# Kernel optimization log

Measured on AMD Instinct MI355X. Metric: run time of the kernel, lower is better.

Reference implementation:

```python
import jax, jax.numpy as jnp
import numpy as np

R_MAX = 5.0
NUM_BASIS = 8
CUTOFF_P = 6
N_LAYERS = 3
C = 64          # hidden_mul / channels of irreps_conv_out (64x0e+64x1o)
Z = 4           # element_number
AVG_DEG = 32.0  # num-neighbor normalization (E/N)
SQRT3 = 1.7320508075688772
SQRT2 = 1.4142135623730951


def _radial_embedding(r):
    # Bessel basis * polynomial cutoff (RadialEdgeEmbedding)
    rs = jnp.maximum(r, 1e-9)
    n = jnp.arange(1, NUM_BASIS + 1, dtype=r.dtype)  # (B,)
    bessel = jnp.sqrt(2.0 / R_MAX) * jnp.sin(n * jnp.pi * rs[:, None] / R_MAX) / rs[:, None]
    x = r / R_MAX
    p = float(CUTOFF_P)
    fc = (1.0
          - (p + 1.0) * (p + 2.0) / 2.0 * x ** CUTOFF_P
          + p * (p + 2.0) * x ** (CUTOFF_P + 1)
          - p * (p + 1.0) / 2.0 * x ** (CUTOFF_P + 2))
    fc = jnp.where(x < 1.0, fc, 0.0)
    return bessel * fc[:, None]  # (E, NUM_BASIS)


def setup_inputs() -> dict:
    key = jax.random.key(0)
    ks = jax.random.split(key, 20)
    N, E, B = 16000, 512000, 16
    atom_type = jax.random.randint(ks[0], (N,), 0, Z)
    # atoms in a 4A box so most edge lengths fall inside r_max=5
    atom_pos = jax.random.uniform(ks[1], (N, 3), dtype=jnp.float32) * 4.0
    edge_src = jax.random.randint(ks[2], (E,), 0, N)
    edge_dst = jax.random.randint(ks[3], (E,), 0, N)
    edge_cell_shift = jnp.zeros((E, 3), jnp.float32)
    cell = jnp.tile(jnp.eye(3, dtype=jnp.float32) * 10.0, (B, 1, 1)) \
        + 0.01 * jax.random.normal(ks[4], (B, 3, 3), jnp.float32)
    image_index = jax.random.randint(ks[5], (N,), 0, B)
    g = lambda k, s, fan: jax.random.normal(k, s, jnp.float32) / np.sqrt(fan)
    return {
        'atom_type': atom_type, 'atom_pos': atom_pos,
        'edge_src': edge_src, 'edge_dst': edge_dst,
        'edge_cell_shift': edge_cell_shift, 'cell': cell, 'image_index': image_index,
        'w_lin_in': g(ks[6], (Z, C), Z),
        'mlp_w1': g(ks[7], (N_LAYERS, NUM_BASIS, 64), NUM_BASIS),
        'mlp_b1': jnp.zeros((N_LAYERS, 64), jnp.float32),
        'mlp_w2': g(ks[8], (N_LAYERS, 64, 5 * C), 64),
        'w_self_s': g(ks[9], (N_LAYERS, C, C), C),
        'w_self_v': g(ks[10], (N_LAYERS, C, C), C),
        'w_gate': g(ks[11], (N_LAYERS, C, C), C),
        'w_lin1': g(ks[12], (C, 16), C),
        'w_lin2': g(ks[13], (16, 1), 16),
    }


def reference(atom_type, atom_pos, edge_src, edge_dst, edge_cell_shift, cell,
              image_index, w_lin_in, mlp_w1, mlp_b1, mlp_w2,
              w_self_s, w_self_v, w_gate, w_lin1, w_lin2):
    N = atom_pos.shape[0]
    # edge vectors with periodic cell shift
    edge_vec = atom_pos[edge_dst] - atom_pos[edge_src]
    edge_vec = edge_vec + jnp.einsum('ni,nij->nj', edge_cell_shift,
                                     cell.reshape(-1, 3, 3)[image_index[edge_src]])
    r = jnp.linalg.norm(edge_vec, axis=1)                      # (E,)
    unit = edge_vec / jnp.maximum(r, 1e-9)[:, None]
    # spherical harmonics lmax=1, component normalization: y0=1 (implicit), y1=sqrt(3)*unit
    y1 = SQRT3 * unit                                           # (E, 3)
    emb = _radial_embedding(r)                                  # (E, NUM_BASIS)

    # one-hot embedding + input linear (one-hot is all 0e -> scalar channels only)
    onehot = jax.nn.one_hot(atom_type, Z, dtype=atom_pos.dtype)
    s = onehot @ w_lin_in                                       # (N, C) l=0 features
    v = jnp.zeros((N, C, 3), atom_pos.dtype)                    # (N, C, 3) l=1 features

    inv_sqrt_deg = 1.0 / np.sqrt(AVG_DEG)
    for L in range(N_LAYERS):
        # radial MLP -> per-edge per-channel tensor-product path weights
        w = jax.nn.silu(emb @ mlp_w1[L] + mlp_b1[L]) @ mlp_w2[L]  # (E, 5C)
        w1, w2, w3, w4, w5 = jnp.split(w, 5, axis=1)              # (E, C) each
        s_src = s[edge_src]                                       # (E, C)
        v_src = v[edge_src]                                       # (E, C, 3)
        vdoty = jnp.einsum('ecx,ex->ec', v_src, y1)
        # CG tensor-product paths (l<=1):
        m_s = w1 * s_src + w2 * vdoty / SQRT3                     # 0x0->0, 1x1->0
        m_v = (w3[:, :, None] * s_src[:, :, None] * y1[:, None, :]      # 0x1->1
               + w4[:, :, None] * v_src                                  # 1x0->1
               + w5[:, :, None] * jnp.cross(v_src, y1[:, None, :]) / SQRT2)  # 1x1->1
        agg_s = jax.ops.segment_sum(m_s, edge_dst, num_segments=N) * inv_sqrt_deg
        agg_v = jax.ops.segment_sum(m_v, edge_dst, num_segments=N) * inv_sqrt_deg
        # gated self-interaction + resnet
        gate = jax.nn.sigmoid(agg_s @ w_gate[L])                  # (N, C)
        s = s + jax.nn.silu(agg_s @ w_self_s[L])
        v = v + jnp.einsum('ncx,cd->ndx', agg_v, w_self_v[L]) * gate[:, :, None]

    # o3.Linear to 16x0e then 1x0e (only scalar channels map to 0e outputs)
    atomic_energy = (s @ w_lin1) @ w_lin2                         # (N, 1)
    atomic_energy = atomic_energy * 1.0                           # atomic_scale
    return atomic_energy
```

## Files before the change

kernel.cpp:

```cpp
#include <hip/hip_runtime.h>
#include <hip/hip_fp16.h>
#include <math.h>

#define NUM_BASIS 8
#define SQRT3 1.7320508075688772f
#define SQRT2 1.4142135623730951f
#define INV_SQRT_DEG 0.17677669529663687f
#define PI_F 3.14159265358979323846f

typedef _Float16 half8 __attribute__((ext_vector_type(8)));
typedef float float4v __attribute__((ext_vector_type(4)));

__device__ __forceinline__ float sigmoidf_(float x) { return 1.0f / (1.0f + __expf(-x)); }
__device__ __forceinline__ float siluf_(float x) { return x * sigmoidf_(x); }

__device__ __forceinline__ void unp2(unsigned u, float& a, float& b) {
    __half2 h = *reinterpret_cast<__half2*>(&u);
    float2 f = __half22float2(h);
    a = f.x; b = f.y;
}
__device__ __forceinline__ unsigned pk2(float a, float b) {
    __half2 h = __floats2half2_rn(a, b);
    return *reinterpret_cast<unsigned*>(&h);
}

__global__ __launch_bounds__(256) void count_deg(
    const int* __restrict__ dst, int* __restrict__ deg, int E)
{
    int base = (blockIdx.x * blockDim.x + threadIdx.x) * 4;
    if (base + 3 < E) {
        int4 d4 = *(const int4*)(dst + base);
        atomicAdd(&deg[d4.x], 1);
        atomicAdd(&deg[d4.y], 1);
        atomicAdd(&deg[d4.z], 1);
        atomicAdd(&deg[d4.w], 1);
    } else {
        for (int e = base; e < E; e++) atomicAdd(&deg[dst[e]], 1);
    }
}

__global__ __launch_bounds__(1024) void scan_deg(
    const int* __restrict__ deg, int* __restrict__ cursor, int N)
{
    __shared__ int wsum[16];
    __shared__ int carry_s, tot_s;
    int tid = threadIdx.x;
    int wid = tid >> 6, lane = tid & 63;
    if (tid == 0) carry_s = 0;
    __syncthreads();
    for (int base = 0; base < N; base += 16384) {
        int i0 = base + tid * 16;
        int v[16];
        int sum = 0;
        #pragma unroll
        for (int k = 0; k < 16; k++) {
            int i = i0 + k;
            v[k] = (i < N) ? deg[i] : 0;
            sum += v[k];
        }
        int incl = sum;
        #pragma unroll
        for (int off = 1; off < 64; off <<= 1) {
            int t = __shfl_up(incl, off);
            if (lane >= off) incl += t;
        }
        if (lane == 63) wsum[wid] = incl;
        __syncthreads();
        if (wid == 0 && lane < 16) {
            int wv = wsum[lane];
            int wincl = wv;
            #pragma unroll
            for (int off = 1; off < 16; off <<= 1) {
                int t = __shfl_up(wincl, off);
                if (lane >= off) wincl += t;
            }
            wsum[lane] = wincl - wv;
            if (lane == 15) tot_s = wincl;
        }
        __syncthreads();
        int carry = carry_s;
        int run = carry + wsum[wid] + incl - sum;
        #pragma unroll
        for (int k = 0; k < 16; k++) {
            int i = i0 + k;
            if (i < N) cursor[i] = run;
            run += v[k];
        }
        __syncthreads();
        if (tid == 0) carry_s = carry + tot_s;
        __syncthreads();
    }
}

__global__ __launch_bounds__(256) void edge_pre_scatter(
    const float* __restrict__ pos, const int* __restrict__ src,
    const int* __restrict__ dst, const float* __restrict__ cs,
    const float* __restrict__ cell, const int* __restrict__ img,
    int* __restrict__ cursor, _Float16* __restrict__ emb,
    uint2* __restrict__ y14, int2* __restrict__ sdp, int E)
{
    int e = blockIdx.x * blockDim.x + threadIdx.x;
    if (e >= E) return;
    int si = src[e], di = dst[e];
    int slot = atomicAdd(&cursor[di], 1);
    sdp[slot] = make_int2(si, di);
    float vx = pos[di*3+0] - pos[si*3+0];
    float vy = pos[di*3+1] - pos[si*3+1];
    float vz = pos[di*3+2] - pos[si*3+2];
    float c0 = cs[(size_t)e*3+0], c1 = cs[(size_t)e*3+1], c2 = cs[(size_t)e*3+2];
    const float* M = cell + (size_t)img[si] * 9;
    vx += c0*M[0] + c1*M[3] + c2*M[6];
    vy += c0*M[1] + c1*M[4] + c2*M[7];
    vz += c0*M[2] + c1*M[5] + c2*M[8];
    float r  = sqrtf(vx*vx + vy*vy + vz*vz);
    float rs = fmaxf(r, 1e-9f);
    float inv = 1.0f / rs;
    uint2 yv;
    yv.x = pk2(SQRT3*vx*inv, SQRT3*vy*inv);
    yv.y = pk2(SQRT3*vz*inv, 0.f);
    y14[slot] = yv;
    float x = r * (1.0f / 5.0f);
    float x2 = x*x, x6 = x2*x2*x2;
    float fc = 1.0f - 28.0f*x6 + 48.0f*x6*x - 21.0f*x6*x2;
    if (x >= 1.0f) fc = 0.0f;
    float pre = sqrtf(2.0f / 5.0f) * inv * fc;
    float t = PI_F * rs * (1.0f / 5.0f);
    half8 ev;
    #pragma unroll
    for (int n = 1; n <= NUM_BASIS; n++)
        ev[n-1] = (_Float16)(pre * __sinf((float)n * t));
    *(half8*)(emb + (size_t)slot*NUM_BASIS) = ev;
}

__global__ __launch_bounds__(256) void prep_weights(
    const float* __restrict__ W2, _Float16* __restrict__ w2f,
    const float* __restrict__ Wg, const float* __restrict__ Ws,
    const float* __restrict__ Wv, _Float16* __restrict__ wgtf,
    const float* __restrict__ Wl1, const float* __restrict__ Wl2,
    float* __restrict__ wl12)
{
    int idx = blockIdx.x * blockDim.x + threadIdx.x;
    if (idx < 64) {
        float a = 0.f;
        #pragma unroll
        for (int j = 0; j < 16; j++) a = fmaf(Wl1[idx*16 + j], Wl2[j], a);
        wl12[idx] = a;
    }
    if (idx < 3 * 20480) {
        int L  = idx / 20480;
        int r  = idx % 20480;
        int cg = r / 5120;
        int r2 = r % 5120;
        int p  = r2 / 1024;
        int r3 = r2 % 1024;
        int kh = r3 / 512;
        int r4 = r3 % 512;
        int lane = r4 / 8;
        int j  = r4 % 8;
        int k = kh*32 + (lane >> 4)*8 + j;
        int n = p*64 + cg*16 + (lane & 15);
        float val = W2[(size_t)L*20480 + k*320 + n];
        if (p == 1)      val *= 0.5773502691896258f;
        else if (p == 4) val *= 0.7071067811865476f;
        w2f[idx] = (_Float16)val;
    } else if (idx < 3*20480 + 3*3*4096) {
        int idx2 = idx - 3*20480;
        int L   = idx2 / 12288;
        int rem = idx2 % 12288;
        int mat = rem / 4096;
        int r2  = rem % 4096;
        int cg  = r2 / 1024;
        int r3  = r2 % 1024;
        int kh  = r3 / 512;
        int r4  = r3 % 512;
        int lane = r4 / 8;
        int j   = r4 % 8;
        int k = kh*32 + (lane >> 4)*8 + j;
        int n = cg*16 + (lane & 15);
        const float* src = (mat == 0) ? Wg : (mat == 1) ? Ws : Wv;
        wgtf[idx2] = (_Float16)src[(size_t)L*4096 + k*64 + n];
    }
}

__global__ __launch_bounds__(256) void mlp1_pre(
    const _Float16* __restrict__ emb, const float* __restrict__ W1,
    const float* __restrict__ B1, _Float16* __restrict__ hA, int E)
{
    int g    = blockIdx.x * blockDim.x + threadIdx.x;
    int kb   = (g & 7) * 8;
    int es   = g >> 3;
    int estr = (gridDim.x * blockDim.x) >> 3;
    float wv[8][8];
    #pragma unroll
    for (int jj = 0; jj < 8; jj++) {
        float4 a = *(const float4*)(W1 + jj*64 + kb);
        float4 b = *(const float4*)(W1 + jj*64 + kb + 4);
        wv[jj][0]=a.x; wv[jj][1]=a.y; wv[jj][2]=a.z; wv[jj][3]=a.w;
        wv[jj][4]=b.x; wv[jj][5]=b.y; wv[jj][6]=b.z; wv[jj][7]=b.w;
    }
    float bv[8];
    {
        float4 a = *(const float4*)(B1 + kb);
        float4 b = *(const float4*)(B1 + kb + 4);
        bv[0]=a.x; bv[1]=a.y; bv[2]=a.z; bv[3]=a.w;
        bv[4]=b.x; bv[5]=b.y; bv[6]=b.z; bv[7]=b.w;
    }
    for (int e = es; e < E; e += estr) {
        half8 ev = *(const half8*)(emb + (size_t)e*8);
        float hv[8];
        #pragma unroll
        for (int j = 0; j < 8; j++) hv[j] = bv[j];
        #pragma unroll
        for (int jj = 0; jj < 8; jj++) {
            float em = (float)ev[jj];
            #pragma unroll
            for (int j = 0; j < 8; j++)
                hv[j] = fmaf(em, wv[jj][j], hv[j]);
        }
        half8 out;
        #pragma unroll
        for (int j = 0; j < 8; j++) out[j] = (_Float16)siluf_(hv[j]);
        *(half8*)(hA + (size_t)e*64 + kb) = out;
    }
}

__device__ __forceinline__ void mlp1_afrag(
    const _Float16* __restrict__ emb, const float* __restrict__ W1,
    const float* __restrict__ B1, int eA, int q, half8 afrag[2])
{
    half8 ev = *(const half8*)(emb + (size_t)eA*8);
    float em[8];
    #pragma unroll
    for (int j = 0; j < 8; j++) em[j] = (float)ev[j];
    #pragma unroll
    for (int kh = 0; kh < 2; kh++) {
        int kb = kh*32 + q*8;
        float hv[8];
        float4 b0 = *(const float4*)(B1 + kb);
        float4 b1 = *(const float4*)(B1 + kb + 4);
        hv[0]=b0.x; hv[1]=b0.y; hv[2]=b0.z; hv[3]=b0.w;
        hv[4]=b1.x; hv[5]=b1.y; hv[6]=b1.z; hv[7]=b1.w;
        #pragma unroll
        for (int jj = 0; jj < 8; jj++) {
            float4 wa = *(const float4*)(W1 + jj*64 + kb);
            float4 wb = *(const float4*)(W1 + jj*64 + kb + 4);
            hv[0] = fmaf(em[jj], wa.x, hv[0]);
            hv[1] = fmaf(em[jj], wa.y, hv[1]);
            hv[2] = fmaf(em[jj], wa.z, hv[2]);
            hv[3] = fmaf(em[jj], wa.w, hv[3]);
            hv[4] = fmaf(em[jj], wb.x, hv[4]);
            hv[5] = fmaf(em[jj], wb.y, hv[5]);
            hv[6] = fmaf(em[jj], wb.z, hv[6]);
            hv[7] = fmaf(em[jj], wb.w, hv[7]);
        }
        #pragma unroll
        for (int j = 0; j < 8; j++)
            afrag[kh][j] = (_Float16)siluf_(hv[j]);
    }
}

template<bool PRE>
__global__ __launch_bounds__(256) void edge_msg_mfma_l0(
    const _Float16* __restrict__ emb, const _Float16* __restrict__ hA,
    const uint2* __restrict__ y14, const int2* __restrict__ sdp,
    const int* __restrict__ type, const float* __restrict__ wlin,
    const float* __restrict__ W1, const float* __restrict__ B1,
    const _Float16* __restrict__ w2f,
    float* __restrict__ aggs, float* __restrict__ aggx,
    float* __restrict__ aggy, float* __restrict__ aggz, int E)
{
    __shared__ _Float16 w2s[8192];
    {
        half8* dstv = (half8*)w2s;
        const half8* srcv = (const half8*)w2f;
        #pragma unroll
        for (int k = 0; k < 4; k++) {
            int t  = threadIdx.x + k*256;
            int cg = t >> 8;
            int r  = t & 255;
            int pp = r >> 7;
            int rk = r & 127;
            dstv[t] = srcv[cg*640 + pp*256 + rk];
        }
    }
    __syncthreads();

    int wave  = (blockIdx.x * blockDim.x + threadIdx.x) >> 6;
    int lane  = threadIdx.x & 63;
    int wbase = wave * 16;
    if (wbase >= E) return;
    int q   = lane >> 4;
    int col = lane & 15;

    half8 afrag[2];
    if (PRE) {
        const _Float16* hp = hA + (size_t)(wbase + col)*64 + q*8;
        afrag[0] = *(const half8*)(hp);
        afrag[1] = *(const half8*)(hp + 32);
    }

    int eb = wbase + q*4;
    int d[4], tt[4];
    float y1x[4], y1y[4], y1z[4];
    #pragma unroll
    for (int r = 0; r < 4; r++) {
        int2 sv = sdp[eb + r];
        tt[r] = type[sv.x];
        d[r]  = sv.y;
        uint2 yv = y14[eb + r];
        float dummy;
        unp2(yv.x, y1x[r], y1y[r]);
        unp2(yv.y, y1z[r], dummy);
    }

    if (!PRE) mlp1_afrag(emb, W1, B1, wbase + col, q, afrag);

    int dnq = __shfl_down(d[0], 16);
    int nd3 = (q == 3) ? -1 : dnq;
    int df = d[0], dl = d[3];
    bool U = (df == dl);
    int dlp = __shfl_up(dl, 16);
    bool link = (q > 0) && (dlp == df);

    #pragma unroll
    for (int cg = 0; cg < 4; cg++) {
        float4v a1 = {0,0,0,0}, a3 = {0,0,0,0};
        const _Float16* wbp = w2s + ((size_t)cg*2048) + (size_t)lane*8;
        {
            half8 b10 = *(const half8*)(wbp + 0*512);
            half8 b11 = *(const half8*)(wbp + 1*512);
            half8 b30 = *(const half8*)(wbp + 2*512);
            half8 b31 = *(const half8*)(wbp + 3*512);
            a1 = __builtin_amdgcn_mfma_f32_16x16x32_f16(afrag[0], b10, a1, 0, 0, 0);
            a1 = __builtin_amdgcn_mfma_f32_16x16x32_f16(afrag[1], b11, a1, 0, 0, 0);
            a3 = __builtin_amdgcn_mfma_f32_16x16x32_f16(afrag[0], b30, a3, 0, 0, 0);
            a3 = __builtin_amdgcn_mfma_f32_16x16x32_f16(afrag[1], b31, a3, 0, 0, 0);
        }
        int c = cg*16 + col;

        float ms[4], mx[4], my[4], mz[4];
        #pragma unroll
        for (int r = 0; r < 4; r++) {
            float s = wlin[tt[r]*64 + c];
            float w3s = a3[r] * s;
            ms[r] = a1[r] * s;
            mx[r] = w3s * y1x[r];
            my[r] = w3s * y1y[r];
            mz[r] = w3s * y1z[r];
        }
        #pragma unroll
        for (int r = 1; r < 4; r++) {
            if (d[r] == d[r-1]) {
                ms[r] += ms[r-1]; mx[r] += mx[r-1];
                my[r] += my[r-1]; mz[r] += mz[r-1];
            }
        }
        float Cs = 0.f, Cx = 0.f, Cy = 0.f, Cz = 0.f;
        #pragma unroll
        for (int it = 0; it < 3; it++) {
            float es = ms[3] + (U ? Cs : 0.f);
            float ex = mx[3] + (U ? Cx : 0.f);
            float ey = my[3] + (U ? Cy : 0.f);
            float ez = mz[3] + (U ? Cz : 0.f);
            float ts = __shfl_up(es, 16);
            float tx = __shfl_up(ex, 16);
            float ty = __shfl_up(ey, 16);
            float tz = __shfl_up(ez, 16);
            Cs = link ? ts : 0.f; Cx = link ? tx : 0.f;
            Cy = link ? ty : 0.f; Cz = link ? tz : 0.f;
        }
        bool hr = true;
        #pragma unroll
        for (int r = 0; r < 4; r++) {
            if (r > 0) hr = hr && (d[r] == d[r-1]);
            float fs = ms[r] + (hr ? Cs : 0.f);
            float fx = mx[r] + (hr ? Cx : 0.f);
            float fy = my[r] + (hr ? Cy : 0.f);
            float fz = mz[r] + (hr ? Cz : 0.f);
            int ndx = (r < 3) ? d[r+1] : nd3;
            if (ndx != d[r] && d[r] >= 0) {
                size_t ai = (size_t)d[r]*64 + c;
                atomicAdd(aggs + ai, fs);
                atomicAdd(aggx + ai, fx);
                atomicAdd(aggy + ai, fy);
                atomicAdd(aggz + ai, fz);
            }
        }
    }
}

__device__ __forceinline__ void process_half(
    const _Float16* __restrict__ w2s, const half8 afrag[2],
    const uint2 pf[4][2], const int d[4], int nd3, bool U, bool link,
    bool live, const float* y1x, const float* y1y, const float* y1z,
    int cgh, int col,
    float* __restrict__ aggs, float* __restrict__ aggx,
    float* __restrict__ aggy, float* __restrict__ aggz)
{
    int lane = threadIdx.x & 63;
    #pragma unroll
    for (int cgl = 0; cgl < 2; cgl++) {
        float4v acc[5];
        #pragma unroll
        for (int p = 0; p < 5; p++) acc[p] = (float4v){0.f, 0.f, 0.f, 0.f};
        const _Float16* wbp = w2s + ((size_t)cgl*5120) + (size_t)lane*8;
        #pragma unroll
        for (int p = 0; p < 5; p++) {
            half8 bf0 = *(const half8*)(wbp + ((size_t)(p*2 + 0))*512);
            half8 bf1 = *(const half8*)(wbp + ((size_t)(p*2 + 1))*512);
            acc[p] = __builtin_amdgcn_mfma_f32_16x16x32_f16(afrag[0], bf0, acc[p], 0, 0, 0);
            acc[p] = __builtin_amdgcn_mfma_f32_16x16x32_f16(afrag[1], bf1, acc[p], 0, 0, 0);
        }
        int c = (cgh*2 + cgl)*16 + col;

        float ms[4], mx[4], my[4], mz[4];
        #pragma unroll
        for (int r = 0; r < 4; r++) {
            float fsx, fvx, fvy, fvz;
            unp2(pf[r][cgl].x, fsx, fvx);
            unp2(pf[r][cgl].y, fvy, fvz);
            float yx = y1x[r], yy = y1y[r], yz = y1z[r];
            float w1 = acc[0][r], w2 = acc[1][r], w3 = acc[2][r];
            float w4 = acc[3][r], w5 = acc[4][r];
            float vdoty = fvx*yx + fvy*yy + fvz*yz;
            ms[r] = fmaf(w1, fsx, w2*vdoty);
            float w3s = w3*fsx;
            float cx = fvy*yz - fvz*yy;
            float cy = fvz*yx - fvx*yz;
            float cz = fvx*yy - fvy*yx;
            mx[r] = fmaf(w3s, yx, fmaf(w4, fvx, w5*cx));
            my[r] = fmaf(w3s, yy, fmaf(w4, fvy, w5*cy));
            mz[r] = fmaf(w3s, yz, fmaf(w4, fvz, w5*cz));
        }
        #pragma unroll
        for (int r = 1; r < 4; r++) {
            if (d[r] == d[r-1]) {
                ms[r] += ms[r-1]; mx[r] += mx[r-1];
                my[r] += my[r-1]; mz[r] += mz[r-1];
            }
        }
        float Cs = 0.f, Cx = 0.f, Cy = 0.f, Cz = 0.f;
        #pragma unroll
        for (int it = 0; it < 3; it++) {
            float es = ms[3] + (U ? Cs : 0.f);
            float ex = mx[3] + (U ? Cx : 0.f);
            float ey = my[3] + (U ? Cy : 0.f);
            float ez = mz[3] + (U ? Cz : 0.f);
            float ts = __shfl_up(es, 16);
            float tx = __shfl_up(ex, 16);
            float ty = __shfl_up(ey, 16);
            float tz = __shfl_up(ez, 16);
            Cs = link ? ts : 0.f; Cx = link ? tx : 0.f;
            Cy = link ? ty : 0.f; Cz = link ? tz : 0.f;
        }
        bool hr = true;
        #pragma unroll
        for (int r = 0; r < 4; r++) {
            if (r > 0) hr = hr && (d[r] == d[r-1]);
            float fs = ms[r] + (hr ? Cs : 0.f);
            float fx = mx[r] + (hr ? Cx : 0.f);
            float fy = my[r] + (hr ? Cy : 0.f);
            float fz = mz[r] + (hr ? Cz : 0.f);
            int ndx = (r < 3) ? d[r+1] : nd3;
            if (ndx != d[r] && d[r] >= 0 && live) {
                size_t ai = (size_t)d[r]*64 + c;
                atomicAdd(aggs + ai, fs);
                atomicAdd(aggx + ai, fx);
                atomicAdd(aggy + ai, fy);
                atomicAdd(aggz + ai, fz);
            }
        }
    }
}

template<bool PRE>
__global__ __launch_bounds__(256) void edge_msg_mfma(
    const _Float16* __restrict__ emb, const _Float16* __restrict__ hA,
    const uint2* __restrict__ y14, const int2* __restrict__ sdp,
    const uint2* __restrict__ nf,
    const float* __restrict__ W1, const float* __restrict__ B1,
    const _Float16* __restrict__ w2f,
    float* __restrict__ aggs, float* __restrict__ aggx,
    float* __restrict__ aggy, float* __restrict__ aggz, int E)
{
    __shared__ _Float16 w2s[10240];
    {
        half8* dstv = (half8*)w2s;
        const half8* srcv = (const half8*)w2f;
        #pragma unroll
        for (int k = 0; k < 5; k++)
            dstv[threadIdx.x + k*256] = srcv[threadIdx.x + k*256];
    }
    __syncthreads();

    int wave  = (blockIdx.x * blockDim.x + threadIdx.x) >> 6;
    int lane  = threadIdx.x & 63;
    int wbase = wave * 16;
    bool live = wbase < E;
    int wb2   = live ? wbase : 0;
    int q   = lane >> 4;
    int col = lane & 15;

    half8 afrag[2];
    if (PRE) {
        const _Float16* hp = hA + (size_t)(wb2 + col)*64 + q*8;
        afrag[0] = *(const half8*)(hp);
        afrag[1] = *(const half8*)(hp + 32);
    }

    int eb = wb2 + q*4;
    int d[4], si[4];
    float y1x[4], y1y[4], y1z[4];
    #pragma unroll
    for (int r = 0; r < 4; r++) {
        int2 sv = sdp[eb + r];
        si[r] = sv.x;
        d[r]  = sv.y;
        uint2 yv = y14[eb + r];
        float dummy;
        unp2(yv.x, y1x[r], y1y[r]);
        unp2(yv.y, y1z[r], dummy);
    }

    uint2 pf[4][2];
    #pragma unroll
    for (int r = 0; r < 4; r++) {
        size_t nb = (size_t)si[r] * 64 + col;
        pf[r][0] = nf[nb];
        pf[r][1] = nf[nb + 16];
    }

    if (!PRE) mlp1_afrag(emb, W1, B1, wb2 + col, q, afrag);

    int dnq = __shfl_down(d[0], 16);
    int nd3 = (q == 3) ? -1 : dnq;
    int df = d[0], dl = d[3];
    bool U = (df == dl);
    int dlp = __shfl_up(dl, 16);
    bool link = (q > 0) && (dlp == df);

    process_half(w2s, afrag, pf, d, nd3, U, link, live,
                 y1x, y1y, y1z, 0, col, aggs, aggx, aggy, aggz);

    #pragma unroll
    for (int r = 0; r < 4; r++) {
        size_t nb = (size_t)si[r] * 64 + 32 + col;
        pf[r][0] = nf[nb];
        pf[r][1] = nf[nb + 16];
    }

    asm volatile("s_waitcnt lgkmcnt(0)" ::: "memory");
    __builtin_amdgcn_s_barrier();
    asm volatile("" ::: "memory");

    {
        half8* dstv = (half8*)w2s;
        const half8* srcv = (const half8*)w2f + 1280;
        #pragma unroll
        for (int k = 0; k < 5; k++)
            dstv[threadIdx.x + k*256] = srcv[threadIdx.x + k*256];
    }

    asm volatile("s_waitcnt lgkmcnt(0)" ::: "memory");
    __builtin_amdgcn_s_barrier();
    asm volatile("" ::: "memory");

    process_half(w2s, afrag, pf, d, nd3, U, link, live,
                 y1x, y1y, y1z, 1, col, aggs, aggx, aggy, aggz);
}

__global__ __launch_bounds__(256) void node_update_mfma(
    uint2* __restrict__ nf,
    float* __restrict__ aggs, float* __restrict__ aggx,
    float* __restrict__ aggy, float* __restrict__ aggz,
    const _Float16* __restrict__ wgtf,
    const int* __restrict__ type, const float* __restrict__ wlin,
    const float* __restrict__ wl12,
    float* __restrict__ out, int first, int do_out, int N)
{
    __shared__ _Float16 wgs[12288];
    {
        half8* dstv = (half8*)wgs;
        const half8* srcv = (const half8*)wgtf;
        #pragma unroll
        for (int k = 0; k < 6; k++)
            dstv[threadIdx.x + k*256] = srcv[threadIdx.x + k*256];
    }

    int wave  = (blockIdx.x * blockDim.x + threadIdx.x) >> 6;
    int lane  = threadIdx.x & 63;
    int wbase = wave * 16;
    bool active = wbase < N;
    int q = lane >> 4, col = lane & 15;

    int nodeA = active ? (wbase + col) : 0;
    if (nodeA >= N) nodeA = N - 1;
    size_t nb = (size_t)nodeA * 64 + q * 8;
    half8 af0[2], af1[2], af2[2], af3[2];
    #pragma unroll
    for (int kh = 0; kh < 2; kh++) {
        const float* p0 = aggs + nb + kh*32;
        const float* p1 = aggx + nb + kh*32;
        const float* p2 = aggy + nb + kh*32;
        const float* p3 = aggz + nb + kh*32;
        float4 a0 = *(const float4*)p0, b0 = *(const float4*)(p0+4);
        float4 a1 = *(const float4*)p1, b1 = *(const float4*)(p1+4);
        float4 a2 = *(const float4*)p2, b2 = *(const float4*)(p2+4);
        float4 a3 = *(const float4*)p3, b3 = *(const float4*)(p3+4);
        af0[kh][0]=(_Float16)(a0.x*INV_SQRT_DEG); af0[kh][1]=(_Float16)(a0.y*INV_SQRT_DEG);
        af0[kh][2]=(_Float16)(a0.z*INV_SQRT_DEG); af0[kh][3]=(_Float16)(a0.w*INV_SQRT_DEG);
        af0[kh][4]=(_Float16)(b0.x*INV_SQRT_DEG); af0[kh][5]=(_Float16)(b0.y*INV_SQRT_DEG);
        af0[kh][6]=(_Float16)(b0.z*INV_SQRT_DEG); af0[kh][7]=(_Float16)(b0.w*INV_SQRT_DEG);
        af1[kh][0]=(_Float16)(a1.x*INV_SQRT_DEG); af1[kh][1]=(_Float16)(a1.y*INV_SQRT_DEG);
        af1[kh][2]=(_Float16)(a1.z*INV_SQRT_DEG); af1[kh][3]=(_Float16)(a1.w*INV_SQRT_DEG);
        af1[kh][4]=(_Float16)(b1.x*INV_SQRT_DEG); af1[kh][5]=(_Float16)(b1.y*INV_SQRT_DEG);
        af1[kh][6]=(_Float16)(b1.z*INV_SQRT_DEG); af1[kh][7]=(_Float16)(b1.w*INV_SQRT_DEG);
        af2[kh][0]=(_Float16)(a2.x*INV_SQRT_DEG); af2[kh][1]=(_Float16)(a2.y*INV_SQRT_DEG);
        af2[kh][2]=(_Float16)(a2.z*INV_SQRT_DEG); af2[kh][3]=(_Float16)(a2.w*INV_SQRT_DEG);
        af2[kh][4]=(_Float16)(b2.x*INV_SQRT_DEG); af2[kh][5]=(_Float16)(b2.y*INV_SQRT_DEG);
        af2[kh][6]=(_Float16)(b2.z*INV_SQRT_DEG); af2[kh][7]=(_Float16)(b2.w*INV_SQRT_DEG);
        af3[kh][0]=(_Float16)(a3.x*INV_SQRT_DEG); af3[kh][1]=(_Float16)(a3.y*INV_SQRT_DEG);
        af3[kh][2]=(_Float16)(a3.z*INV_SQRT_DEG); af3[kh][3]=(_Float16)(a3.w*INV_SQRT_DEG);
        af3[kh][4]=(_Float16)(b3.x*INV_SQRT_DEG); af3[kh][5]=(_Float16)(b3.y*INV_SQRT_DEG);
        af3[kh][6]=(_Float16)(b3.z*INV_SQRT_DEG); af3[kh][7]=(_Float16)(b3.w*INV_SQRT_DEG);
    }

    int tt[4];
    #pragma unroll
    for (int r = 0; r < 4; r++) {
        int nd = wbase + q*4 + r;
        tt[r] = type[(active && nd < N) ? nd : 0];
    }

    __syncthreads();

    float epart[4] = {0.f, 0.f, 0.f, 0.f};

    #pragma unroll
    for (int cg = 0; cg < 4; cg++) {
        const _Float16* bp = wgs + (size_t)lane * 8;
        half8 bg0 = *(const half8*)(bp + ((size_t)((0*4 + cg)*2 + 0))*512);
        half8 bg1 = *(const half8*)(bp + ((size_t)((0*4 + cg)*2 + 1))*512);
        half8 bs0 = *(const half8*)(bp + ((size_t)((1*4 + cg)*2 + 0))*512);
        half8 bs1 = *(const half8*)(bp + ((size_t)((1*4 + cg)*2 + 1))*512);
        half8 bv0 = *(const half8*)(bp + ((size_t)((2*4 + cg)*2 + 0))*512);
        half8 bv1 = *(const half8*)(bp + ((size_t)((2*4 + cg)*2 + 1))*512);
        float4v ag = {0,0,0,0}, as = {0,0,0,0};
        float4v ox = {0,0,0,0}, oy = {0,0,0,0}, oz = {0,0,0,0};
        ag = __builtin_amdgcn_mfma_f32_16x16x32_f16(af0[0], bg0, ag, 0, 0, 0);
        ag = __builtin_amdgcn_mfma_f32_16x16x32_f16(af0[1], bg1, ag, 0, 0, 0);
        as = __builtin_amdgcn_mfma_f32_16x16x32_f16(af0[0], bs0, as, 0, 0, 0);
        as = __builtin_amdgcn_mfma_f32_16x16x32_f16(af0[1], bs1, as, 0, 0, 0);
        ox = __builtin_amdgcn_mfma_f32_16x16x32_f16(af1[0], bv0, ox, 0, 0, 0);
        ox = __builtin_amdgcn_mfma_f32_16x16x32_f16(af1[1], bv1, ox, 0, 0, 0);
        oy = __builtin_amdgcn_mfma_f32_16x16x32_f16(af2[0], bv0, oy, 0, 0, 0);
        oy = __builtin_amdgcn_mfma_f32_16x16x32_f16(af2[1], bv1, oy, 0, 0, 0);
        oz = __builtin_amdgcn_mfma_f32_16x16x32_f16(af3[0], bv0, oz, 0, 0, 0);
        oz = __builtin_amdgcn_mfma_f32_16x16x32_f16(af3[1], bv1, oz, 0, 0, 0);

        if (!active) continue;
        int c = cg*16 + col;
        float wlc = wl12[c];
        #pragma unroll
        for (int r = 0; r < 4; r++) {
            int nd = wbase + q*4 + r;
            bool wr = nd < N;
            size_t ni = (size_t)nd*64 + c;
            float sx, vx, vy, vz;
            if (first) {
                sx = wlin[tt[r]*64 + c];
                vx = 0.f; vy = 0.f; vz = 0.f;
            } else {
                uint2 cur = nf[wr ? ni : 0];
                unp2(cur.x, sx, vx);
                unp2(cur.y, vy, vz);
            }
            float gate = sigmoidf_(ag[r]);
            sx += siluf_(as[r]);
            vx += ox[r] * gate;
            vy += oy[r] * gate;
            vz += oz[r] * gate;
            if (wr) {
                uint2 nv;
                nv.x = pk2(sx, vx);
                nv.y = pk2(vy, vz);
                nf[ni] = nv;
                aggs[ni] = 0.f;
                aggx[ni] = 0.f;
                aggy[ni] = 0.f;
                aggz[ni] = 0.f;
                epart[r] = fmaf(sx, wlc, epart[r]);
            }
        }
    }
    if (do_out && active) {
        #pragma unroll
        for (int r = 0; r < 4; r++) {
            float e = epart[r];
            e += __shfl_xor(e, 1);
            e += __shfl_xor(e, 2);
            e += __shfl_xor(e, 4);
            e += __shfl_xor(e, 8);
            int nd = wbase + q*4 + r;
            if (col == 0 && nd < N) out[nd] = e;
        }
    }
}

extern "C" void kernel_launch(void* const* d_in, const int* in_sizes, int n_in,
                              void* d_out, int out_size, void* d_ws, size_t ws_size,
                              hipStream_t stream)
{
    const int*   atom_type = (const int*)  d_in[0];
    const float* pos       = (const float*)d_in[1];
    const int*   src       = (const int*)  d_in[2];
    const int*   dst       = (const int*)  d_in[3];
    const float* cs        = (const float*)d_in[4];
    const float* cell      = (const float*)d_in[5];
    const int*   img       = (const int*)  d_in[6];
    const float* wlin_in   = (const float*)d_in[7];
    const float* mw1       = (const float*)d_in[8];
    const float* mb1       = (const float*)d_in[9];
    const float* mw2       = (const float*)d_in[10];
    const float* wss       = (const float*)d_in[11];
    const float* wsv       = (const float*)d_in[12];
    const float* wg        = (const float*)d_in[13];
    const float* wl1       = (const float*)d_in[14];
    const float* wl2       = (const float*)d_in[15];
    int N = in_sizes[0];
    int E = in_sizes[2];

    char* w = (char*)d_ws;
    _Float16* emb = (_Float16*)w; w += (size_t)E * 8 * sizeof(_Float16);
    uint2*  y14  = (uint2*)w;  w += (size_t)E * sizeof(uint2);
    int2*   sdp  = (int2*)w;   w += (size_t)E * sizeof(int2);
    uint2*  nf   = (uint2*)w;  w += (size_t)N * 64 * sizeof(uint2);
    float*  agg  = (float*)w;  w += (size_t)N * 64 * 4 * sizeof(float);
    _Float16* w2f  = (_Float16*)w; w += (size_t)3 * 20480 * sizeof(_Float16);
    _Float16* wgtf = (_Float16*)w; w += (size_t)3 * 3 * 4096 * sizeof(_Float16);
    float*  wl12 = (float*)w;  w += 64 * sizeof(float);
    int*    deg  = (int*)w;    w += (size_t)N * sizeof(int);
    int*    curs = (int*)w;    w += (size_t)N * sizeof(int);

    size_t used   = (size_t)(w - (char*)d_ws);
    size_t hbytes = (size_t)E * 64 * sizeof(_Float16);
    int nh = (ws_size >= used + hbytes) ? 1 : 0;
    _Float16* hbuf = (_Float16*)w;

    size_t NC = (size_t)N * 64;
    float* aggs = agg;
    float* aggx = agg + NC;
    float* aggy = agg + 2*NC;
    float* aggz = agg + 3*NC;

    hipMemsetAsync(deg, 0, (size_t)N * sizeof(int), stream);
    hipMemsetAsync(agg, 0, NC * 4 * sizeof(float), stream);
    count_deg<<<(E/4 + 255) / 256, 256, 0, stream>>>(dst, deg, E);
    scan_deg<<<1, 1024, 0, stream>>>(deg, curs, N);
    int prep_n = 3*20480 + 3*3*4096;
    prep_weights<<<(prep_n + 255) / 256, 256, 0, stream>>>(
        mw2, w2f, wg, wss, wsv, wgtf, wl1, wl2, wl12);
    edge_pre_scatter<<<(E + 255) / 256, 256, 0, stream>>>(
        pos, src, dst, cs, cell, img, curs, emb, y14, sdp, E);

    int eblocks = (E + 63) / 64;
    int nblocks = (N + 63) / 64;
    int pblocks = 2048;

    if (nh) {
        mlp1_pre<<<pblocks, 256, 0, stream>>>(emb, mw1, mb1, hbuf, E);
        edge_msg_mfma_l0<true><<<eblocks, 256, 0, stream>>>(
            emb, hbuf, y14, sdp, atom_type, wlin_in,
            mw1, mb1, w2f, aggs, aggx, aggy, aggz, E);
    } else {
        edge_msg_mfma_l0<false><<<eblocks, 256, 0, stream>>>(
            emb, nullptr, y14, sdp, atom_type, wlin_in,
            mw1, mb1, w2f, aggs, aggx, aggy, aggz, E);
    }
    node_update_mfma<<<nblocks, 256, 0, stream>>>(
        nf, aggs, aggx, aggy, aggz, wgtf, atom_type, wlin_in, wl12,
        (float*)d_out, 1, 0, N);

    for (int L = 1; L < 3; L++) {
        if (nh) {
            mlp1_pre<<<pblocks, 256, 0, stream>>>(
                emb, mw1 + L * 8 * 64, mb1 + L * 64, hbuf, E);
            edge_msg_mfma<true><<<eblocks, 256, 0, stream>>>(
                emb, hbuf, y14, sdp, nf,
                mw1 + L * 8 * 64, mb1 + L * 64, w2f + (size_t)L * 20480,
                aggs, aggx, aggy, aggz, E);
        } else {
            edge_msg_mfma<false><<<eblocks, 256, 0, stream>>>(
                emb, nullptr, y14, sdp, nf,
                mw1 + L * 8 * 64, mb1 + L * 64, w2f + (size_t)L * 20480,
                aggs, aggx, aggy, aggz, E);
        }
        node_update_mfma<<<nblocks, 256, 0, stream>>>(
            nf, aggs, aggx, aggy, aggz,
            wgtf + (size_t)L * 12288, atom_type, wlin_in, wl12,
            (float*)d_out, 0, (L == 2) ? 1 : 0, N);
    }
}
```

Measured before the change: 464.9 us.

## Fuse weight prep into scan, overlap next-layer MLP1 with node update, uniform-dst fast path

Merges the degree scan and weight preparation into one launch, with extra blocks doing the weight conversion. The next layer's MLP1 precompute is now run by extra blocks of the node-update kernel, so it overlaps with node work and needs no separate launch. In the edge message kernels, when all 16 edges of a wave share one destination, a cross-lane shuffle reduction does a single atomic per channel instead of the segmented reduction. The overlap depends on the hidden-buffer reuse being ordered correctly, and the uniform-destination check adds a wave vote to every wave.

```diff
diff --git a/kernel.cpp b/kernel.cpp
--- a/kernel.cpp
+++ b/kernel.cpp
@@ -39,9 +39,59 @@
     }
 }
 
-__global__ __launch_bounds__(1024) void scan_deg(
-    const int* __restrict__ deg, int* __restrict__ cursor, int N)
-{
+__global__ __launch_bounds__(1024) void scan_prep(
+    const int* __restrict__ deg, int* __restrict__ cursor, int N,
+    const float* __restrict__ W2, _Float16* __restrict__ w2f,
+    const float* __restrict__ Wg, const float* __restrict__ Ws,
+    const float* __restrict__ Wv, _Float16* __restrict__ wgtf,
+    const float* __restrict__ Wl1, const float* __restrict__ Wl2,
+    float* __restrict__ wl12)
+{
+    if (blockIdx.x != 0) {
+        int idx = ((int)blockIdx.x - 1) * 1024 + (int)threadIdx.x;
+        if (idx < 64) {
+            float a = 0.f;
+            #pragma unroll
+            for (int j = 0; j < 16; j++) a = fmaf(Wl1[idx*16 + j], Wl2[j], a);
+            wl12[idx] = a;
+        }
+        if (idx < 3 * 20480) {
+            int L  = idx / 20480;
+            int r  = idx % 20480;
+            int cg = r / 5120;
+            int r2 = r % 5120;
+            int p  = r2 / 1024;
+            int r3 = r2 % 1024;
+            int kh = r3 / 512;
+            int r4 = r3 % 512;
+            int lane = r4 / 8;
+            int j  = r4 % 8;
+            int k = kh*32 + (lane >> 4)*8 + j;
+            int n = p*64 + cg*16 + (lane & 15);
+            float val = W2[(size_t)L*20480 + k*320 + n];
+            if (p == 1)      val *= 0.5773502691896258f;
+            else if (p == 4) val *= 0.7071067811865476f;
+            w2f[idx] = (_Float16)val;
+        } else if (idx < 3*20480 + 3*3*4096) {
+            int idx2 = idx - 3*20480;
+            int L   = idx2 / 12288;
+            int rem = idx2 % 12288;
+            int mat = rem / 4096;
+            int r2  = rem % 4096;
+            int cg  = r2 / 1024;
+            int r3  = r2 % 1024;
+            int kh  = r3 / 512;
+            int r4  = r3 % 512;
+            int lane = r4 / 8;
+            int j   = r4 % 8;
+            int k = kh*32 + (lane >> 4)*8 + j;
+            int n = cg*16 + (lane & 15);
+            const float* src = (mat == 0) ? Wg : (mat == 1) ? Ws : Wv;
+            wgtf[idx2] = (_Float16)src[(size_t)L*4096 + k*64 + n];
+        }
+        return;
+    }
+
     __shared__ int wsum[16];
     __shared__ int carry_s, tot_s;
     int tid = threadIdx.x;
@@ -132,64 +182,14 @@
     *(half8*)(emb + (size_t)slot*NUM_BASIS) = ev;
 }
 
-__global__ __launch_bounds__(256) void prep_weights(
-    const float* __restrict__ W2, _Float16* __restrict__ w2f,
-    const float* __restrict__ Wg, const float* __restrict__ Ws,
-    const float* __restrict__ Wv, _Float16* __restrict__ wgtf,
-    const float* __restrict__ Wl1, const float* __restrict__ Wl2,
-    float* __restrict__ wl12)
-{
-    int idx = blockIdx.x * blockDim.x + threadIdx.x;
-    if (idx < 64) {
-        float a = 0.f;
-        #pragma unroll
-        for (int j = 0; j < 16; j++) a = fmaf(Wl1[idx*16 + j], Wl2[j], a);
-        wl12[idx] = a;
-    }
-    if (idx < 3 * 20480) {
-        int L  = idx / 20480;
-        int r  = idx % 20480;
-        int cg = r / 5120;
-        int r2 = r % 5120;
-        int p  = r2 / 1024;
-        int r3 = r2 % 1024;
-        int kh = r3 / 512;
-        int r4 = r3 % 512;
-        int lane = r4 / 8;
-        int j  = r4 % 8;
-        int k = kh*32 + (lane >> 4)*8 + j;
-        int n = p*64 + cg*16 + (lane & 15);
-        float val = W2[(size_t)L*20480 + k*320 + n];
-        if (p == 1)      val *= 0.5773502691896258f;
-        else if (p == 4) val *= 0.7071067811865476f;
-        w2f[idx] = (_Float16)val;
-    } else if (idx < 3*20480 + 3*3*4096) {
-        int idx2 = idx - 3*20480;
-        int L   = idx2 / 12288;
-        int rem = idx2 % 12288;
-        int mat = rem / 4096;
-        int r2  = rem % 4096;
-        int cg  = r2 / 1024;
-        int r3  = r2 % 1024;
-        int kh  = r3 / 512;
-        int r4  = r3 % 512;
-        int lane = r4 / 8;
-        int j   = r4 % 8;
-        int k = kh*32 + (lane >> 4)*8 + j;
-        int n = cg*16 + (lane & 15);
-        const float* src = (mat == 0) ? Wg : (mat == 1) ? Ws : Wv;
-        wgtf[idx2] = (_Float16)src[(size_t)L*4096 + k*64 + n];
-    }
-}
-
-__global__ __launch_bounds__(256) void mlp1_pre(
+__device__ __forceinline__ void mlp1_pre_body(
     const _Float16* __restrict__ emb, const float* __restrict__ W1,
-    const float* __restrict__ B1, _Float16* __restrict__ hA, int E)
-{
-    int g    = blockIdx.x * blockDim.x + threadIdx.x;
+    const float* __restrict__ B1, _Float16* __restrict__ hA, int E,
+    int g, int nthreads)
+{
     int kb   = (g & 7) * 8;
     int es   = g >> 3;
-    int estr = (gridDim.x * blockDim.x) >> 3;
+    int estr = nthreads >> 3;
     float wv[8][8];
     #pragma unroll
     for (int jj = 0; jj < 8; jj++) {
@@ -222,6 +222,14 @@
         for (int j = 0; j < 8; j++) out[j] = (_Float16)siluf_(hv[j]);
         *(half8*)(hA + (size_t)e*64 + kb) = out;
     }
+}
+
+__global__ __launch_bounds__(256) void mlp1_pre(
+    const _Float16* __restrict__ emb, const float* __restrict__ W1,
+    const float* __restrict__ B1, _Float16* __restrict__ hA, int E)
+{
+    int g = blockIdx.x * blockDim.x + threadIdx.x;
+    mlp1_pre_body(emb, W1, B1, hA, E, g, gridDim.x * blockDim.x);
 }
 
 __device__ __forceinline__ void mlp1_afrag(
@@ -314,6 +322,9 @@
     }
 
     if (!PRE) mlp1_afrag(emb, W1, B1, wbase + col, q, afrag);
+
+    int dfirst = __shfl(d[0], 0);
+    bool uni = __all(d[3] == dfirst);
 
     int dnq = __shfl_down(d[0], 16);
     int nd3 = (q == 3) ? -1 : dnq;
@@ -348,6 +359,26 @@
             my[r] = w3s * y1y[r];
             mz[r] = w3s * y1z[r];
         }
+
+        if (uni) {
+            float fs = (ms[0]+ms[1]) + (ms[2]+ms[3]);
+            float fx = (mx[0]+mx[1]) + (mx[2]+mx[3]);
+            float fy = (my[0]+my[1]) + (my[2]+my[3]);
+            float fz = (mz[0]+mz[1]) + (mz[2]+mz[3]);
+            fs += __shfl_xor(fs, 16); fx += __shfl_xor(fx, 16);
+            fy += __shfl_xor(fy, 16); fz += __shfl_xor(fz, 16);
+            fs += __shfl_xor(fs, 32); fx += __shfl_xor(fx, 32);
+            fy += __shfl_xor(fy, 32); fz += __shfl_xor(fz, 32);
+            if (q == 0) {
+                size_t ai = (size_t)d[0]*64 + c;
+                atomicAdd(aggs + ai, fs);
+                atomicAdd(aggx + ai, fx);
+                atomicAdd(aggy + ai, fy);
+                atomicAdd(aggz + ai, fz);
+            }
+            continue;
+        }
+
         #pragma unroll
         for (int r = 1; r < 4; r++) {
             if (d[r] == d[r-1]) {
@@ -392,12 +423,14 @@
 __device__ __forceinline__ void process_half(
     const _Float16* __restrict__ w2s, const half8 afrag[2],
     const uint2 pf[4][2], const int d[4], int nd3, bool U, bool link,
-    bool live, const float* y1x, const float* y1y, const float* y1z,
+    bool uni, bool live,
+    const float* y1x, const float* y1y, const float* y1z,
     int cgh, int col,
     float* __restrict__ aggs, float* __restrict__ aggx,
     float* __restrict__ aggy, float* __restrict__ aggz)
 {
     int lane = threadIdx.x & 63;
+    int q = lane >> 4;
     #pragma unroll
     for (int cgl = 0; cgl < 2; cgl++) {
         float4v acc[5];
@@ -432,6 +465,26 @@
             my[r] = fmaf(w3s, yy, fmaf(w4, fvy, w5*cy));
             mz[r] = fmaf(w3s, yz, fmaf(w4, fvz, w5*cz));
         }
+
+        if (uni) {
+            float fs = (ms[0]+ms[1]) + (ms[2]+ms[3]);
+            float fx = (mx[0]+mx[1]) + (mx[2]+mx[3]);
+            float fy = (my[0]+my[1]) + (my[2]+my[3]);
+            float fz = (mz[0]+mz[1]) + (mz[2]+mz[3]);
+            fs += __shfl_xor(fs, 16); fx += __shfl_xor(fx, 16);
+            fy += __shfl_xor(fy, 16); fz += __shfl_xor(fz, 16);
+            fs += __shfl_xor(fs, 32); fx += __shfl_xor(fx, 32);
+            fy += __shfl_xor(fy, 32); fz += __shfl_xor(fz, 32);
+            if (q == 0 && live) {
+                size_t ai = (size_t)d[0]*64 + c;
+                atomicAdd(aggs + ai, fs);
+                atomicAdd(aggx + ai, fx);
+                atomicAdd(aggy + ai, fy);
+                atomicAdd(aggz + ai, fz);
+            }
+            continue;
+        }
+
         #pragma unroll
         for (int r = 1; r < 4; r++) {
             if (d[r] == d[r-1]) {
@@ -532,6 +585,9 @@
 
     if (!PRE) mlp1_afrag(emb, W1, B1, wb2 + col, q, afrag);
 
+    int dfirst = __shfl(d[0], 0);
+    bool uni = __all(d[3] == dfirst);
+
     int dnq = __shfl_down(d[0], 16);
     int nd3 = (q == 3) ? -1 : dnq;
     int df = d[0], dl = d[3];
@@ -539,7 +595,7 @@
     int dlp = __shfl_up(dl, 16);
     bool link = (q > 0) && (dlp == df);
 
-    process_half(w2s, afrag, pf, d, nd3, U, link, live,
+    process_half(w2s, afrag, pf, d, nd3, U, link, uni, live,
                  y1x, y1y, y1z, 0, col, aggs, aggx, aggy, aggz);
 
     #pragma unroll
@@ -565,7 +621,7 @@
     __builtin_amdgcn_s_barrier();
     asm volatile("" ::: "memory");
 
-    process_half(w2s, afrag, pf, d, nd3, U, link, live,
+    process_half(w2s, afrag, pf, d, nd3, U, link, uni, live,
                  y1x, y1y, y1z, 1, col, aggs, aggx, aggy, aggz);
 }
 
@@ -576,8 +632,18 @@
     const _Float16* __restrict__ wgtf,
     const int* __restrict__ type, const float* __restrict__ wlin,
     const float* __restrict__ wl12,
-    float* __restrict__ out, int first, int do_out, int N)
-{
+    float* __restrict__ out, int first, int do_out, int N,
+    const _Float16* __restrict__ emb, const float* __restrict__ W1n,
+    const float* __restrict__ B1n, _Float16* __restrict__ hA, int E,
+    int nb_node)
+{
+    if ((int)blockIdx.x >= nb_node) {
+        int g = ((int)blockIdx.x - nb_node) * 256 + (int)threadIdx.x;
+        mlp1_pre_body(emb, W1n, B1n, hA, E, g,
+                      ((int)gridDim.x - nb_node) * 256);
+        return;
+    }
+
     __shared__ _Float16 wgs[12288];
     {
         half8* dstv = (half8*)wgs;
@@ -756,10 +822,9 @@
     hipMemsetAsync(deg, 0, (size_t)N * sizeof(int), stream);
     hipMemsetAsync(agg, 0, NC * 4 * sizeof(float), stream);
     count_deg<<<(E/4 + 255) / 256, 256, 0, stream>>>(dst, deg, E);
-    scan_deg<<<1, 1024, 0, stream>>>(deg, curs, N);
     int prep_n = 3*20480 + 3*3*4096;
-    prep_weights<<<(prep_n + 255) / 256, 256, 0, stream>>>(
-        mw2, w2f, wg, wss, wsv, wgtf, wl1, wl2, wl12);
+    scan_prep<<<1 + (prep_n + 1023) / 1024, 1024, 0, stream>>>(
+        deg, curs, N, mw2, w2f, wg, wss, wsv, wgtf, wl1, wl2, wl12);
     edge_pre_scatter<<<(E + 255) / 256, 256, 0, stream>>>(
         pos, src, dst, cs, cell, img, curs, emb, y14, sdp, E);
 
@@ -777,14 +842,13 @@
             emb, nullptr, y14, sdp, atom_type, wlin_in,
             mw1, mb1, w2f, aggs, aggx, aggy, aggz, E);
     }
-    node_update_mfma<<<nblocks, 256, 0, stream>>>(
+    node_update_mfma<<<nblocks + (nh ? pblocks : 0), 256, 0, stream>>>(
         nf, aggs, aggx, aggy, aggz, wgtf, atom_type, wlin_in, wl12,
-        (float*)d_out, 1, 0, N);
+        (float*)d_out, 1, 0, N,
+        emb, mw1 + 1 * 8 * 64, mb1 + 1 * 64, hbuf, E, nblocks);
 
     for (int L = 1; L < 3; L++) {
         if (nh) {
-            mlp1_pre<<<pblocks, 256, 0, stream>>>(
-                emb, mw1 + L * 8 * 64, mb1 + L * 64, hbuf, E);
             edge_msg_mfma<true><<<eblocks, 256, 0, stream>>>(
                 emb, hbuf, y14, sdp, nf,
                 mw1 + L * 8 * 64, mb1 + L * 64, w2f + (size_t)L * 20480,
@@ -795,9 +859,13 @@
                 mw1 + L * 8 * 64, mb1 + L * 64, w2f + (size_t)L * 20480,
                 aggs, aggx, aggy, aggz, E);
         }
-        node_update_mfma<<<nblocks, 256, 0, stream>>>(
+        int fuse = (nh && L < 2) ? pblocks : 0;
+        node_update_mfma<<<nblocks + fuse, 256, 0, stream>>>(
             nf, aggs, aggx, aggy, aggz,
             wgtf + (size_t)L * 12288, atom_type, wlin_in, wl12,
-            (float*)d_out, 0, (L == 2) ? 1 : 0, N);
-    }
-}
+            (float*)d_out, 0, (L == 2) ? 1 : 0, N,
+            emb, mw1 + (L+1 < 3 ? L+1 : 0) * 8 * 64,
+            mb1 + (L+1 < 3 ? L+1 : 0) * 64, hbuf, E,
+            fuse ? nblocks : (nblocks + fuse + 1));
+    }
+}
```

Measured after the change: 450.0 us. 1.03x faster.
